# Optimization experiments

Measured on AMD Instinct MI355X. Metric: run time of the kernel, lower is better.

## Reference

```python
import jax, jax.numpy as jnp
import numpy as np

B, L = 128, 128            # batch, num_features (sequence length)
D_MODEL = 256
D_INNER = 512              # expand=2
D_STATE = 16
D_CONV = 4
DT_RANK = 16               # ceil(d_model/16)
N_LAYERS = 2
LN_EPS = 1e-5


def setup_inputs() -> dict:
    key = jax.random.key(0)
    ks = jax.random.split(key, 12)
    rn = lambda k, shp, s=0.02: (jax.random.normal(k, shp, jnp.float32) * s)
    A_init = jnp.tile(jnp.arange(1, D_STATE + 1, dtype=jnp.float32), (N_LAYERS, D_INNER, 1))
    return {
        "x_num": jax.random.normal(ks[0], (B, L), jnp.float32),
        "scalar_w": rn(ks[1], (D_MODEL, 1), 0.5),
        "scalar_b": jnp.zeros((D_MODEL,), jnp.float32),
        "in_proj_w": rn(ks[2], (N_LAYERS, 2 * D_INNER, D_MODEL)),
        "conv_w": rn(ks[3], (N_LAYERS, D_INNER, D_CONV), 0.2),
        "conv_b": jnp.zeros((N_LAYERS, D_INNER), jnp.float32),
        "x_proj_w": rn(ks[4], (N_LAYERS, DT_RANK + 2 * D_STATE, D_INNER)),
        "dt_proj_w": rn(ks[5], (N_LAYERS, D_INNER, DT_RANK), 0.1),
        "dt_proj_b": jnp.full((N_LAYERS, D_INNER), float(np.log(np.expm1(0.01))), jnp.float32),
        "A_log": jnp.log(A_init),
        "D_skip": jnp.ones((N_LAYERS, D_INNER), jnp.float32),
        "out_proj_w": rn(ks[6], (N_LAYERS, D_MODEL, D_INNER)),
        "ln_g": jnp.ones((D_MODEL,), jnp.float32),
        "ln_b": jnp.zeros((D_MODEL,), jnp.float32),
        "h1_w": rn(ks[7], (D_MODEL, D_MODEL)),
        "h1_b": jnp.zeros((D_MODEL,), jnp.float32),
        "h2_w": rn(ks[8], (1, D_MODEL)),
        "h2_b": jnp.zeros((1,), jnp.float32),
    }


def _selective_scan(u, delta, A, Bm, C, D_skip):
    # u, delta: [B,L,Di]; A: [Di,N]; Bm, C: [B,L,N]
    deltaA = jnp.exp(jnp.einsum('bld,dn->bldn', delta, A))          # [B,L,Di,N]
    deltaBu = jnp.einsum('bld,bln,bld->bldn', delta, Bm, u)          # [B,L,Di,N]
    h0 = jnp.zeros((u.shape[0], u.shape[2], A.shape[1]), u.dtype)

    def step(h, inp):
        dA_t, dBu_t, c_t = inp
        h = dA_t * h + dBu_t                                         # [B,Di,N]
        y = jnp.einsum('bdn,bn->bd', h, c_t)
        return h, y

    _, ys = jax.lax.scan(
        step, h0,
        (deltaA.transpose(1, 0, 2, 3), deltaBu.transpose(1, 0, 2, 3), C.transpose(1, 0, 2)))
    return ys.transpose(1, 0, 2) + u * D_skip                        # [B,L,Di]


def _mamba_block(x, Wi, cw, cb, Wx, Wdt, bdt, A_log, Dsk, Wo):
    xz = jnp.einsum('bld,ed->ble', x, Wi)                            # [B,L,2*Di]
    xh, z = jnp.split(xz, 2, axis=-1)
    # causal depthwise conv1d, kernel D_CONV
    xt = xh.transpose(0, 2, 1)                                       # [B,Di,L]
    conv = jax.lax.conv_general_dilated(
        xt, cw[:, None, :], window_strides=(1,), padding=[(D_CONV - 1, 0)],
        feature_group_count=D_INNER)
    xh = jax.nn.silu((conv + cb[:, None]).transpose(0, 2, 1))        # [B,L,Di]
    x_dbl = jnp.einsum('bld,ed->ble', xh, Wx)                        # [B,L,DT_RANK+2N]
    dt, Bm, C = jnp.split(x_dbl, [DT_RANK, DT_RANK + D_STATE], axis=-1)
    delta = jax.nn.softplus(jnp.einsum('blr,dr->bld', dt, Wdt) + bdt)
    A = -jnp.exp(A_log)
    y = _selective_scan(xh, delta, A, Bm, C, Dsk)
    y = y * jax.nn.silu(z)
    return jnp.einsum('bld,od->blo', y, Wo)                          # [B,L,D_MODEL]


def reference(x_num, scalar_w, scalar_b, in_proj_w, conv_w, conv_b, x_proj_w,
              dt_proj_w, dt_proj_b, A_log, D_skip, out_proj_w, ln_g, ln_b,
              h1_w, h1_b, h2_w, h2_b):
    # scalar_proj: Linear(1, d_model) applied to each feature value
    x = x_num[:, :, None] * scalar_w[:, 0] + scalar_b                # [B,L,D_MODEL]
    for i in range(N_LAYERS):
        x = _mamba_block(x, in_proj_w[i], conv_w[i], conv_b[i], x_proj_w[i],
                         dt_proj_w[i], dt_proj_b[i], A_log[i], D_skip[i], out_proj_w[i])
    mu = x.mean(-1, keepdims=True)
    var = ((x - mu) ** 2).mean(-1, keepdims=True)
    x = (x - mu) * jax.lax.rsqrt(var + LN_EPS) * ln_g + ln_b
    pooled = x.mean(axis=1)                                          # [B,D_MODEL]
    h = jax.nn.gelu(pooled @ h1_w.T + h1_b, approximate=False)
    return (h @ h2_w.T + h2_b)[:, 0]                                 # [B]
```

## Files before the change

### kernel.cpp

```cpp
#include <hip/hip_runtime.h>
#include <math.h>

#define BB 128
#define LL 128
#define DM 256
#define DI 512
#define NS 16
#define MR (BB*LL)
#define SC 8
#define ST 16
#define EPAD 34

typedef unsigned short u16;
typedef __attribute__((ext_vector_type(8))) short bf16x8;
typedef __attribute__((ext_vector_type(8))) short us8;
typedef __attribute__((ext_vector_type(4))) short u16x4;
typedef __attribute__((ext_vector_type(4))) float f32x4;
typedef __attribute__((ext_vector_type(2))) float f32x2;

__device__ __forceinline__ u16 f2bf(float v) {
    unsigned u = __float_as_uint(v);
    return (u16)((u + 0x7fffu + ((u >> 16) & 1u)) >> 16);
}
__device__ __forceinline__ u16 ftoh(float v) {
    _Float16 h = (_Float16)v;
    return __builtin_bit_cast(unsigned short, h);
}
__device__ __forceinline__ float htof(u16 x) {
    return (float)__builtin_bit_cast(_Float16, x);
}

__device__ __forceinline__ void g2l16(const u16* g, u16* l) {
    __builtin_amdgcn_global_load_lds(
        (const __attribute__((address_space(1))) void*)g,
        (__attribute__((address_space(3))) void*)l,
        16, 0, 0);
}

__device__ __forceinline__ void unpack8(const f32x4& a, const f32x4& b,
                                        const f32x4& c, const f32x4& d, f32x2* o) {
    o[0]=(f32x2){a[0],a[1]}; o[1]=(f32x2){a[2],a[3]};
    o[2]=(f32x2){b[0],b[1]}; o[3]=(f32x2){b[2],b[3]};
    o[4]=(f32x2){c[0],c[1]}; o[5]=(f32x2){c[2],c[3]};
    o[6]=(f32x2){d[0],d[1]}; o[7]=(f32x2){d[2],d[3]};
}

__device__ __forceinline__ void pow_tree2(float r, f32x2* p2) {
    float q = r*r, s = q*q, t = s*s;
    p2[0] = (f32x2){r, q};
    f32x2 qq = (f32x2){q, q}, ss = (f32x2){s, s}, tt = (f32x2){t, t};
    p2[1] = p2[0]*qq;
    p2[2] = p2[0]*ss;
    p2[3] = p2[1]*ss;
    p2[4] = p2[0]*tt;
    p2[5] = p2[1]*tt;
    p2[6] = p2[2]*tt;
    p2[7] = p2[3]*tt;
}

__device__ __forceinline__ void store8h(const float* v, u16* dh) {
    bf16x8 hv;
    #pragma unroll
    for (int j = 0; j < 8; j++) hv[j] = (short)f2bf(v[j]);
    *(bf16x8*)dh = hv;
}

__device__ __forceinline__ void unswz(int id, int NB, int& nb, int& mb) {
    int low = id & 7, rest = id >> 3;
    nb = rest % NB;
    mb = ((rest / NB) << 3) | low;
}

#define NCI (1024*32)
#define NCP (640*64)
#define NCO (256*64)
#define REG (NCI+NCP+NCO)
#define WSET 1441792
__global__ __launch_bounds__(256) void k_prep(
    const float* __restrict__ xn, const float* __restrict__ sw, const float* __restrict__ sbias,
    const float* __restrict__ Wi_all, const float* __restrict__ Wx_all,
    const float* __restrict__ Wdt_all, const float* __restrict__ Wo_all,
    u16* __restrict__ wbase, u16* __restrict__ AhA)
{
    int gc = blockIdx.x * 256 + threadIdx.x;
    if (gc < 2*REG) {
        int layer = (gc >= REG) ? 1 : 0;
        int c0 = gc - layer*REG;
        u16* wb = wbase + (size_t)layer*WSET;
        const float* Wi  = Wi_all  + (size_t)layer*1024*256;
        const float* Wx  = Wx_all  + (size_t)layer*48*512;
        const float* Wdt = Wdt_all + (size_t)layer*512*16;
        const float* Wo  = Wo_all  + (size_t)layer*256*512;
        float v[8];
        u16* dh;
        if (c0 < NCI) {
            int c = c0, m = c & 127, t = c >> 7, kc = t & 31, rb = t >> 5;
            const float* p = Wi + (size_t)(rb*128 + m)*256 + kc*8;
            float4 a = *(const float4*)p, b = *(const float4*)(p+4);
            v[0]=a.x; v[1]=a.y; v[2]=a.z; v[3]=a.w; v[4]=b.x; v[5]=b.y; v[6]=b.z; v[7]=b.w;
            dh = wb + (size_t)c*8;
        } else if (c0 < NCI + NCP) {
            int c = c0 - NCI, m = c & 127, t = c >> 7, kc = t & 63, rb = t >> 6;
            int row = rb*128 + m, k0 = kc*8;
            if (row < 512) {
                #pragma unroll
                for (int j = 0; j < 8; j++) v[j] = 0.f;
                #pragma unroll
                for (int r = 0; r < 16; r++) {
                    float wv = Wdt[row*16 + r];
                    const float* p = Wx + r*512 + k0;
                    #pragma unroll
                    for (int j = 0; j < 8; j++) v[j] += wv * p[j];
                }
            } else if (row < 544) {
                const float* p = Wx + (size_t)(row - 496)*512 + k0;
                #pragma unroll
                for (int j = 0; j < 8; j++) v[j] = p[j];
            } else {
                #pragma unroll
                for (int j = 0; j < 8; j++) v[j] = 0.f;
            }
            dh = wb + 524288 + (size_t)c*8;
        } else {
            int c = c0 - NCI - NCP, m = c & 127, t = c >> 7, kc = t & 63, rb = t >> 6;
            const float* p = Wo + (size_t)(rb*128 + m)*512 + kc*8;
            float4 a = *(const float4*)p, b = *(const float4*)(p+4);
            v[0]=a.x; v[1]=a.y; v[2]=a.z; v[3]=a.w; v[4]=b.x; v[5]=b.y; v[6]=b.z; v[7]=b.w;
            dh = wb + 1179648 + (size_t)c*8;
        }
        store8h(v, dh);
    } else {
        int id = gc - 2*REG;
        int row = id & (MR - 1);
        int kc  = id >> 14;
        float v = xn[row];
        float4 w0 = ((const float4*)sw)[kc*2],    w1 = ((const float4*)sw)[kc*2+1];
        float4 b0 = ((const float4*)sbias)[kc*2], b1 = ((const float4*)sbias)[kc*2+1];
        float vals[8] = { v*w0.x+b0.x, v*w0.y+b0.y, v*w0.z+b0.z, v*w0.w+b0.w,
                          v*w1.x+b1.x, v*w1.y+b1.y, v*w1.z+b1.z, v*w1.w+b1.w };
        size_t c = ((size_t)(row >> 7) * 32 + kc) * 128 + (row & 127);
        store8h(vals, &AhA[c*8]);
    }
}

template<int CM>
__global__ __launch_bounds__(256) void k_gemm_mfma(
    const u16* __restrict__ Ah, const u16* __restrict__ Bh,
    void* __restrict__ Cv, void* __restrict__ C2v,
    const float* __restrict__ bdt,
    int K, int Nvalid, int nsplit, int ldc, int ldc2, int NB)
{
    __shared__ __align__(16) u16 sAh[2][4*128*8];
    __shared__ __align__(16) u16 sBh[2][4*64*8];

    const int tid = threadIdx.x, lane = tid & 63, w = tid >> 6;
    const int wm = w >> 1, wn = w & 1;
    const int r16 = lane & 15, quad = lane >> 4;
    int nb, mb;
    unswz(blockIdx.x, NB, nb, mb);
    const int K8 = K >> 3;
    const int NT = K >> 5;

    f32x4 acc[4][2];
    #pragma unroll
    for (int mt = 0; mt < 4; mt++)
        #pragma unroll
        for (int nt = 0; nt < 2; nt++) acc[mt][nt] = (f32x4){0.f,0.f,0.f,0.f};

    const u16* gAh = Ah + (size_t)mb * K8 * 128 * 8;
    const int rbB = nb >> 1, boff = (nb & 1) * 64;
    const u16* gBh = Bh + (size_t)rbB * K8 * 128 * 8;

    {
        #pragma unroll
        for (int t = 0; t < 2; t++) {
            int s = w + t * 4;
            g2l16(gAh + (size_t)(s*64 + lane)*8, &sAh[0][(s*64 + lane)*8]);
        }
        g2l16(gBh + ((size_t)w*128 + boff + lane)*8, &sBh[0][(w*64 + lane)*8]);
    }

    int cur = 0;
    for (int t = 0; t < NT; t++) {
        __syncthreads();
        if (t + 1 < NT) {
            const int kc0 = (t + 1) * 4;
            const u16* ga = gAh + (size_t)kc0 * 128 * 8;
            int nx = cur ^ 1;
            #pragma unroll
            for (int tt = 0; tt < 2; tt++) {
                int s = w + tt * 4;
                g2l16(ga + (size_t)(s*64 + lane)*8, &sAh[nx][(s*64 + lane)*8]);
            }
            g2l16(gBh + ((size_t)(kc0 + w)*128 + boff + lane)*8, &sBh[nx][(w*64 + lane)*8]);
        }

        bf16x8 fa_h[4], fb_h[2];
        #pragma unroll
        for (int mt = 0; mt < 4; mt++) {
            int ch = quad*128 + wm*64 + mt*16 + r16;
            fa_h[mt] = *(const bf16x8*)&sAh[cur][ch*8];
        }
        #pragma unroll
        for (int nt = 0; nt < 2; nt++) {
            int ch = quad*64 + wn*32 + nt*16 + r16;
            fb_h[nt] = *(const bf16x8*)&sBh[cur][ch*8];
        }
        #pragma unroll
        for (int mt = 0; mt < 4; mt++)
            #pragma unroll
            for (int nt = 0; nt < 2; nt++)
                acc[mt][nt] = __builtin_amdgcn_mfma_f32_16x16x32_bf16(fa_h[mt], fb_h[nt], acc[mt][nt], 0, 0, 0);
        cur ^= 1;
    }

    const int col0 = nb*64 + wn*32;
    #pragma unroll
    for (int mt = 0; mt < 4; mt++) {
        int lrow = wm*64 + mt*16 + quad*4;
        int rowb = mb*128 + lrow;
        #pragma unroll
        for (int nt = 0; nt < 2; nt++) {
            int col = col0 + nt*16 + r16;
            if (col < Nvalid) {
                if (CM != 2 && col >= nsplit) {
                    float* Cd = (float*)C2v; int cc = col - nsplit;
                    #pragma unroll
                    for (int r = 0; r < 4; r++)
                        Cd[(size_t)(rowb + r)*ldc2 + cc] = acc[mt][nt][r];
                } else if (CM == 1) {
                    u16* Cd = (u16*)Cv;
                    float bv = bdt[col];
                    u16x4 pd;
                    #pragma unroll
                    for (int r = 0; r < 4; r++) {
                        float v    = acc[mt][nt][r] + bv;
                        float expv = __expf(v);
                        float dlt  = (v > 20.f) ? v : __logf(1.f + expv);
                        pd[r] = (short)ftoh(dlt);
                    }
                    *(u16x4*)&Cd[((size_t)mb*512 + col)*128 + lrow] = pd;
                } else if (CM == 2) {
                    u16* Dh = (u16*)Cv;
                    size_t cb = ((size_t)mb*32 + (col>>3))*1024 + (col&7);
                    #pragma unroll
                    for (int r = 0; r < 4; r++)
                        Dh[cb + (size_t)(lrow + r)*8] = f2bf(acc[mt][nt][r]);
                } else {
                    float* Cd = (float*)Cv;
                    #pragma unroll
                    for (int r = 0; r < 4; r++)
                        Cd[(size_t)(rowb + r)*ldc + col] = acc[mt][nt][r];
                }
            }
        }
    }
}

__global__ __launch_bounds__(256) void k_gemm_in(
    const u16* __restrict__ Ah, const u16* __restrict__ Bh,
    const float* __restrict__ cw, const float* __restrict__ cb,
    u16* __restrict__ Yh, u16* __restrict__ u2, u16* __restrict__ z2)
{
    __shared__ __align__(16) char smem[24576];
    u16* sAh = (u16*)smem;
    u16* sBh = (u16*)(smem + 16384);

    const int tid = threadIdx.x, lane = tid & 63, w = tid >> 6;
    const int wm = w >> 1, wn = w & 1;
    const int r16 = lane & 15, quad = lane >> 4;
    int nb, mb;
    unswz(blockIdx.x, 16, nb, mb);
    const int K8 = 32;
    const int NT = 8;

    f32x4 acc[4][2];
    #pragma unroll
    for (int mt = 0; mt < 4; mt++)
        #pragma unroll
        for (int nt = 0; nt < 2; nt++) acc[mt][nt] = (f32x4){0.f,0.f,0.f,0.f};

    const u16* gAh = Ah + (size_t)mb * K8 * 128 * 8;
    const int rbB = nb >> 1, boff = (nb & 1) * 64;
    const u16* gBh = Bh + (size_t)rbB * K8 * 128 * 8;

    {
        #pragma unroll
        for (int t = 0; t < 2; t++) {
            int s = w + t * 4;
            g2l16(gAh + (size_t)(s*64 + lane)*8, &sAh[(s*64 + lane)*8]);
        }
        g2l16(gBh + ((size_t)w*128 + boff + lane)*8, &sBh[(w*64 + lane)*8]);
    }

    int cur = 0;
    for (int t = 0; t < NT; t++) {
        __syncthreads();
        if (t + 1 < NT) {
            const int kc0 = (t + 1) * 4;
            const u16* ga = gAh + (size_t)kc0 * 128 * 8;
            u16* dA = sAh + (cur ^ 1) * 4096;
            u16* dB = sBh + (cur ^ 1) * 2048;
            #pragma unroll
            for (int tt = 0; tt < 2; tt++) {
                int s = w + tt * 4;
                g2l16(ga + (size_t)(s*64 + lane)*8, &dA[(s*64 + lane)*8]);
            }
            g2l16(gBh + ((size_t)(kc0 + w)*128 + boff + lane)*8, &dB[(w*64 + lane)*8]);
        }

        const u16* rA = sAh + cur * 4096;
        const u16* rB = sBh + cur * 2048;
        bf16x8 fa_h[4], fb_h[2];
        #pragma unroll
        for (int mt = 0; mt < 4; mt++) {
            int ch = quad*128 + wm*64 + mt*16 + r16;
            fa_h[mt] = *(const bf16x8*)&rA[ch*8];
        }
        #pragma unroll
        for (int nt = 0; nt < 2; nt++) {
            int ch = quad*64 + wn*32 + nt*16 + r16;
            fb_h[nt] = *(const bf16x8*)&rB[ch*8];
        }
        #pragma unroll
        for (int mt = 0; mt < 4; mt++)
            #pragma unroll
            for (int nt = 0; nt < 2; nt++)
                acc[mt][nt] = __builtin_amdgcn_mfma_f32_16x16x32_bf16(fa_h[mt], fb_h[nt], acc[mt][nt], 0, 0, 0);
        cur ^= 1;
    }

    if (nb < 8) {
        float* eps = (float*)smem;
        float* scw = (float*)(smem + 17408);
        float* scb = (float*)(smem + 18432);
        __syncthreads();
        if (tid < 256) scw[tid] = cw[nb*256 + tid];
        if (tid < 64)  scb[tid] = cb[nb*64 + tid];

        #pragma unroll
        for (int rr = 0; rr < 2; rr++) {
            if (wn == rr) {
                #pragma unroll
                for (int mt = 0; mt < 4; mt++) {
                    int rbase = wm*64 + mt*16 + quad*4;
                    #pragma unroll
                    for (int ntl = 0; ntl < 2; ntl++) {
                        int ct = ntl*16 + r16;
                        #pragma unroll
                        for (int r = 0; r < 4; r++)
                            eps[(rbase + r)*EPAD + ct] = acc[mt][ntl][r];
                    }
                }
            }
            __syncthreads();
            #pragma unroll
            for (int t = 0; t < 2; t++) {
                int l  = (tid & 31) + ((tid >> 5) & 3) * 32;
                int oo = (tid >> 7) + t*2;
                int dl_ = rr*32 + oo*8;
                float xr[4][8];
                #pragma unroll
                for (int r2 = 0; r2 < 4; r2++) {
                    int row = l - 3 + r2;
                    if (row >= 0) {
                        const float2* p = (const float2*)&eps[row*EPAD + oo*8];
                        float2 a = p[0], b2 = p[1], c2 = p[2], d2 = p[3];
                        xr[r2][0]=a.x; xr[r2][1]=a.y; xr[r2][2]=b2.x; xr[r2][3]=b2.y;
                        xr[r2][4]=c2.x; xr[r2][5]=c2.y; xr[r2][6]=d2.x; xr[r2][7]=d2.y;
                    } else {
                        #pragma unroll
                        for (int j = 0; j < 8; j++) xr[r2][j] = 0.f;
                    }
                }
                float uv[8];
                #pragma unroll
                for (int j = 0; j < 8; j++) {
                    int dj = dl_ + j;
                    float4 w4 = *(const float4*)&scw[dj*4];
                    float s = scb[dj] + w4.x*xr[0][j] + w4.y*xr[1][j]
                                      + w4.z*xr[2][j] + w4.w*xr[3][j];
                    float sig = 1.f/(1.f + __expf(-s));
                    uv[j] = s*sig;
                }
                int d = nb*64 + dl_;
                size_t base = ((size_t)(mb*64 + (d>>3))*128 + l)*8;
                store8h(uv, &Yh[base]);
                #pragma unroll
                for (int j = 0; j < 8; j++)
                    u2[((size_t)mb*512 + d + j)*128 + l] = ftoh(uv[j]);
            }
            __syncthreads();
        }
    } else {
        const int col0 = (nb-8)*64 + wn*32;
        #pragma unroll
        for (int mt = 0; mt < 4; mt++) {
            int lb = wm*64 + mt*16 + quad*4;
            #pragma unroll
            for (int nt = 0; nt < 2; nt++) {
                int d = col0 + nt*16 + r16;
                u16x4 pk;
                #pragma unroll
                for (int r = 0; r < 4; r++) pk[r] = (short)ftoh(acc[mt][nt][r]);
                *(u16x4*)&z2[((size_t)mb*512 + d)*128 + lb] = pk;
            }
        }
    }
}

__global__ __launch_bounds__(512, 8) void k_scan_fused(
    const u16* __restrict__ dls, const float* __restrict__ bc,
    const u16* __restrict__ uu, const u16* __restrict__ zz,
    const float* __restrict__ Dsk, u16* __restrict__ Yh)
{
    __shared__ float sR[SC][64];
    __shared__ float sH[SC][64*17];
    const int tid  = threadIdx.x;
    const int lane = tid & 63;
    const int c    = __builtin_amdgcn_readfirstlane(tid >> 6);
    const int dgrp = blockIdx.x & 7;
    const int b    = blockIdx.x >> 3;
    const int d    = dgrp*64 + lane;
    const int l0   = c*ST;

    const float dsk = Dsk[d];
    const size_t tb = ((size_t)b*512 + d)*128 + l0;
    const u16* pd = dls + tb;
    const u16* up = uu + tb;
    const u16* zp = zz + tb;
    const size_t ybase = ((size_t)(b*64 + (d>>3))*128 + l0)*8 + (d&7);
    const float* bp = bc + ((size_t)b*LL + l0)*32;

    f32x2 h2[8];
    #pragma unroll
    for (int n = 0; n < 8; n++) h2[n] = (f32x2){0.f, 0.f};
    float R = 1.f;

    #pragma unroll 1
    for (int t8 = 0; t8 < ST/8; t8++) {
        us8 vd = *(const us8*)(pd + t8*8);
        us8 vu = *(const us8*)(up + t8*8);
        #pragma unroll
        for (int j = 0; j < 8; j++) {
            int t = t8*8 + j;
            const float* bpt = bp + t*32;
            f32x4 qa = *(const f32x4*)(bpt);
            f32x4 qb = *(const f32x4*)(bpt + 4);
            f32x4 qc = *(const f32x4*)(bpt + 8);
            f32x4 qd = *(const f32x4*)(bpt + 12);
            f32x2 bvv[8];
            unpack8(qa, qb, qc, qd, bvv);
            float dlt = htof((u16)vd[j]);
            float r1  = __expf(-dlt);
            float du  = dlt * htof((u16)vu[j]);
            R *= r1;
            f32x2 p2[8];
            pow_tree2(r1, p2);
            f32x2 du2 = (f32x2){du, du};
            #pragma unroll
            for (int n = 0; n < 8; n++) h2[n] = p2[n]*h2[n] + bvv[n]*du2;
        }
    }

    sR[c][lane] = R;
    #pragma unroll
    for (int n = 0; n < 8; n++) {
        sH[c][lane*17 + 2*n]     = h2[n][0];
        sH[c][lane*17 + 2*n + 1] = h2[n][1];
    }
    __syncthreads();
    f32x2 hin2[8];
    #pragma unroll
    for (int n = 0; n < 8; n++) hin2[n] = (f32x2){0.f, 0.f};
    for (int cc = 0; cc < c; cc++) {
        float Rv = sR[cc][lane];
        f32x2 P2[8];
        pow_tree2(Rv, P2);
        #pragma unroll
        for (int n = 0; n < 8; n++) {
            f32x2 Sv = (f32x2){sH[cc][lane*17 + 2*n], sH[cc][lane*17 + 2*n + 1]};
            hin2[n] = P2[n]*hin2[n] + Sv;
        }
    }

    #pragma unroll
    for (int n = 0; n < 8; n++) h2[n] = hin2[n];

    u16* ph = Yh + ybase;

    #pragma unroll 1
    for (int t8 = 0; t8 < ST/8; t8++) {
        us8 vd = *(const us8*)(pd + t8*8);
        us8 vu = *(const us8*)(up + t8*8);
        us8 vz = *(const us8*)(zp + t8*8);
        #pragma unroll
        for (int j = 0; j < 8; j++) {
            int t = t8*8 + j;
            const float* bpt = bp + t*32;
            f32x4 qa = *(const f32x4*)(bpt);
            f32x4 qb = *(const f32x4*)(bpt + 4);
            f32x4 qc = *(const f32x4*)(bpt + 8);
            f32x4 qd = *(const f32x4*)(bpt + 12);
            f32x4 qe = *(const f32x4*)(bpt + 16);
            f32x4 qf = *(const f32x4*)(bpt + 20);
            f32x4 qg = *(const f32x4*)(bpt + 24);
            f32x4 qh = *(const f32x4*)(bpt + 28);
            f32x2 bvv[8], cvv[8];
            unpack8(qa, qb, qc, qd, bvv);
            unpack8(qe, qf, qg, qh, cvv);
            float dlt = htof((u16)vd[j]);
            float r1  = __expf(-dlt);
            float u   = htof((u16)vu[j]);
            float zv  = htof((u16)vz[j]);
            float du  = dlt * u;
            f32x2 p2[8];
            pow_tree2(r1, p2);
            f32x2 du2 = (f32x2){du, du};
            f32x2 yv2 = (f32x2){0.f, 0.f};
            #pragma unroll
            for (int n = 0; n < 8; n++) {
                h2[n] = p2[n]*h2[n] + bvv[n]*du2;
                yv2  += h2[n]*cvv[n];
            }
            float yv = yv2[0] + yv2[1] + u * dsk;
            float sig = 1.f/(1.f + __expf(-zv));
            float yg = yv * (zv * sig);
            ph[(size_t)t*8] = f2bf(yg);
        }
    }
}

__global__ __launch_bounds__(256) void k_ln_head(const float* __restrict__ x,
    const float* __restrict__ g, const float* __restrict__ bt,
    const float* __restrict__ h1w, const float* __restrict__ h1b,
    const float* __restrict__ h2w, const float* __restrict__ h2b,
    float* __restrict__ out)
{
    __shared__ float4 part[4][64];
    __shared__ float sp[DM];
    __shared__ float sred[DM];
    int b = blockIdx.x, tid = threadIdx.x, wave = tid >> 6, lane = tid & 63;
    const float4* xp = (const float4*)(x + (size_t)b*LL*DM);
    float4 acc = make_float4(0.f, 0.f, 0.f, 0.f);
    for (int i = 0; i < 32; i++) {
        int l = wave*32 + i;
        float4 v = xp[l*64 + lane];
        float s  = v.x + v.y + v.z + v.w;
        float s2 = v.x*v.x + v.y*v.y + v.z*v.z + v.w*v.w;
        #pragma unroll
        for (int off = 32; off > 0; off >>= 1) {
            s  += __shfl_down(s,  off, 64);
            s2 += __shfl_down(s2, off, 64);
        }
        s  = __shfl(s,  0, 64);
        s2 = __shfl(s2, 0, 64);
        float mu  = s  * (1.f/DM);
        float var = s2 * (1.f/DM) - mu*mu;
        float rs  = rsqrtf(var + 1e-5f);
        acc.x += (v.x - mu)*rs;
        acc.y += (v.y - mu)*rs;
        acc.z += (v.z - mu)*rs;
        acc.w += (v.w - mu)*rs;
    }
    part[wave][lane] = acc;
    __syncthreads();
    if (wave == 0) {
        float4 a0 = part[0][lane], a1 = part[1][lane], a2 = part[2][lane], a3 = part[3][lane];
        float4 gv = ((const float4*)g)[lane];
        float4 bv = ((const float4*)bt)[lane];
        float4 o;
        o.x = (a0.x+a1.x+a2.x+a3.x)*(1.f/LL)*gv.x + bv.x;
        o.y = (a0.y+a1.y+a2.y+a3.y)*(1.f/LL)*gv.y + bv.y;
        o.z = (a0.z+a1.z+a2.z+a3.z)*(1.f/LL)*gv.z + bv.z;
        o.w = (a0.w+a1.w+a2.w+a3.w)*(1.f/LL)*gv.w + bv.w;
        *(float4*)&sp[lane*4] = o;
    }
    __syncthreads();
    int j = tid;
    float a = h1b[j];
    const float* wr = &h1w[(size_t)j*DM];
    for (int m = 0; m < DM; m += 4) {
        float4 w4 = *(const float4*)&wr[m];
        a += sp[m]*w4.x + sp[m+1]*w4.y + sp[m+2]*w4.z + sp[m+3]*w4.w;
    }
    float hg = 0.5f*a*(1.f + erff(a*0.70710678118654752440f));
    sred[j] = hg * h2w[j];
    __syncthreads();
    for (int s = 128; s > 0; s >>= 1) {
        if (j < s) sred[j] += sred[j+s];
        __syncthreads();
    }
    if (j == 0) out[b] = sred[0] + h2b[0];
}

extern "C" void kernel_launch(void* const* d_in, const int* in_sizes, int n_in,
                              void* d_out, int out_size, void* d_ws, size_t ws_size,
                              hipStream_t stream)
{
    const float* x_num    = (const float*)d_in[0];
    const float* scalar_w = (const float*)d_in[1];
    const float* scalar_b = (const float*)d_in[2];
    const float* in_proj  = (const float*)d_in[3];
    const float* conv_w   = (const float*)d_in[4];
    const float* conv_b   = (const float*)d_in[5];
    const float* x_proj   = (const float*)d_in[6];
    const float* dt_w     = (const float*)d_in[7];
    const float* dt_b     = (const float*)d_in[8];
    const float* D_skip   = (const float*)d_in[10];
    const float* out_proj = (const float*)d_in[11];
    const float* ln_g     = (const float*)d_in[12];
    const float* ln_b     = (const float*)d_in[13];
    const float* h1_w     = (const float*)d_in[14];
    const float* h1_b     = (const float*)d_in[15];
    const float* h2_w     = (const float*)d_in[16];
    const float* h2_b     = (const float*)d_in[17];
    float* out = (float*)d_out;

    float* ws      = (float*)d_ws;
    float* x_buf   = ws;
    float* xh_raw  = x_buf  + (size_t)MR*DM;
    float* z_buf   = xh_raw + (size_t)MR*DI;
    float* xh      = z_buf  + (size_t)MR*DI;
    float* xdbl    = xh     + (size_t)MR*DI;
    float* wsplit  = xdbl   + (size_t)MR*48;

    u16* AhA = (u16*)xh;
    u16* u2  = (u16*)(xh + (size_t)MR*256);
    u16* AhX = (u16*)xh_raw;
    u16* z2  = (u16*)z_buf;
    u16* dl2 = (u16*)x_buf;
    float* bc = xdbl;

    u16* wbase = (u16*)wsplit;

    const int BIG = 1 << 30;

    k_prep<<<(2*REG + MR*32)/256, 256, 0, stream>>>(
        x_num, scalar_w, scalar_b, in_proj, x_proj, dt_w, out_proj,
        wbase, AhA);

    for (int layer = 0; layer < 2; layer++) {
        u16* wb  = wbase + (size_t)layer*WSET;
        u16* WhI = wb;
        u16* WhP = wb + 524288;
        u16* WhO = wb + 1179648;

        k_gemm_in<<<16*BB, 256, 0, stream>>>(
            AhA, WhI,
            conv_w + (size_t)layer*DI*4, conv_b + (size_t)layer*DI,
            AhX, u2, z2);

        k_gemm_mfma<1><<<9*BB, 256, 0, stream>>>(
            AhX, WhP, (void*)dl2, (void*)bc,
            dt_b + (size_t)layer*DI, 512, 544, 512, 512, 32, 9);

        k_scan_fused<<<BB*8, 512, 0, stream>>>(dl2, bc, u2, z2,
            D_skip + (size_t)layer*DI, AhX);

        if (layer == 0)
            k_gemm_mfma<2><<<4*BB, 256, 0, stream>>>(
                AhX, WhO, (void*)AhA, (void*)0, (const float*)0,
                512, 256, BIG, 256, 256, 4);
        else
            k_gemm_mfma<0><<<4*BB, 256, 0, stream>>>(
                AhX, WhO, x_buf, x_buf, (const float*)0,
                512, 256, BIG, 256, 256, 4);
    }

    k_ln_head<<<BB, 256, 0, stream>>>(x_buf, ln_g, ln_b, h1_w, h1_b, h2_w, h2_b, out);
}
```

Before: 314.8 us.

## Fold scalar projection into layer-0 in_proj and fuse out_proj0 into in_proj1

The layer-0 in_proj GEMM is replaced by a rank-1 closed form. Because the input is x*w+b, in_proj(x) = x*(Wi·w) + (Wi·b), so a new front kernel computes conv and SiLU directly from per-channel vectors. The layer-0 out_proj and the layer-1 in_proj are merged into a single 512-K GEMM with precomputed combined weights Wi1·Wo0, which removes one full activation GEMM pass. The cost is a small weight-weight GEMM per call and a change in bf16 rounding, since the combined weight product is rounded once instead of the intermediate activations.

```diff
diff --git a/kernel.cpp b/kernel.cpp
--- a/kernel.cpp
+++ b/kernel.cpp
@@ -74,72 +74,145 @@
 #define NCI (1024*32)
 #define NCP (640*64)
 #define NCO (256*64)
-#define REG (NCI+NCP+NCO)
-#define WSET 1441792
+#define NPREP (NCI + 2*NCP + 2*NCO + 256)
+#define OFF_WI1  0
+#define OFF_WP0  262144
+#define OFF_WP1  589824
+#define OFF_WO1  917504
+#define OFF_WOT0 1048576
 __global__ __launch_bounds__(256) void k_prep(
-    const float* __restrict__ xn, const float* __restrict__ sw, const float* __restrict__ sbias,
+    const float* __restrict__ sw, const float* __restrict__ sbias,
     const float* __restrict__ Wi_all, const float* __restrict__ Wx_all,
     const float* __restrict__ Wdt_all, const float* __restrict__ Wo_all,
-    u16* __restrict__ wbase, u16* __restrict__ AhA)
+    u16* __restrict__ wbase, float* __restrict__ wvbv)
 {
     int gc = blockIdx.x * 256 + threadIdx.x;
-    if (gc < 2*REG) {
-        int layer = (gc >= REG) ? 1 : 0;
-        int c0 = gc - layer*REG;
-        u16* wb = wbase + (size_t)layer*WSET;
-        const float* Wi  = Wi_all  + (size_t)layer*1024*256;
+    float v[8];
+    u16* dh;
+    if (gc < NCI) {
+        int c = gc, m = c & 127, t = c >> 7, kc = t & 31, rb = t >> 5;
+        const float* Wi = Wi_all + (size_t)1024*256;
+        const float* p = Wi + (size_t)(rb*128 + m)*256 + kc*8;
+        float4 a = *(const float4*)p, b = *(const float4*)(p+4);
+        v[0]=a.x; v[1]=a.y; v[2]=a.z; v[3]=a.w; v[4]=b.x; v[5]=b.y; v[6]=b.z; v[7]=b.w;
+        dh = wbase + OFF_WI1 + (size_t)c*8;
+    } else if (gc < NCI + 2*NCP) {
+        int g = gc - NCI;
+        int layer = (g >= NCP) ? 1 : 0;
+        int c = g - layer*NCP;
         const float* Wx  = Wx_all  + (size_t)layer*48*512;
         const float* Wdt = Wdt_all + (size_t)layer*512*16;
-        const float* Wo  = Wo_all  + (size_t)layer*256*512;
-        float v[8];
-        u16* dh;
-        if (c0 < NCI) {
-            int c = c0, m = c & 127, t = c >> 7, kc = t & 31, rb = t >> 5;
-            const float* p = Wi + (size_t)(rb*128 + m)*256 + kc*8;
-            float4 a = *(const float4*)p, b = *(const float4*)(p+4);
-            v[0]=a.x; v[1]=a.y; v[2]=a.z; v[3]=a.w; v[4]=b.x; v[5]=b.y; v[6]=b.z; v[7]=b.w;
-            dh = wb + (size_t)c*8;
-        } else if (c0 < NCI + NCP) {
-            int c = c0 - NCI, m = c & 127, t = c >> 7, kc = t & 63, rb = t >> 6;
-            int row = rb*128 + m, k0 = kc*8;
-            if (row < 512) {
+        int m = c & 127, t = c >> 7, kc = t & 63, rb = t >> 6;
+        int row = rb*128 + m, k0 = kc*8;
+        if (row < 512) {
+            #pragma unroll
+            for (int j = 0; j < 8; j++) v[j] = 0.f;
+            #pragma unroll
+            for (int r = 0; r < 16; r++) {
+                float wvx = Wdt[row*16 + r];
+                const float* p = Wx + r*512 + k0;
                 #pragma unroll
-                for (int j = 0; j < 8; j++) v[j] = 0.f;
-                #pragma unroll
-                for (int r = 0; r < 16; r++) {
-                    float wv = Wdt[row*16 + r];
-                    const float* p = Wx + r*512 + k0;
-                    #pragma unroll
-                    for (int j = 0; j < 8; j++) v[j] += wv * p[j];
-                }
-            } else if (row < 544) {
-                const float* p = Wx + (size_t)(row - 496)*512 + k0;
-                #pragma unroll
-                for (int j = 0; j < 8; j++) v[j] = p[j];
-            } else {
-                #pragma unroll
-                for (int j = 0; j < 8; j++) v[j] = 0.f;
-            }
-            dh = wb + 524288 + (size_t)c*8;
+                for (int j = 0; j < 8; j++) v[j] += wvx * p[j];
+            }
+        } else if (row < 544) {
+            const float* p = Wx + (size_t)(row - 496)*512 + k0;
+            #pragma unroll
+            for (int j = 0; j < 8; j++) v[j] = p[j];
         } else {
-            int c = c0 - NCI - NCP, m = c & 127, t = c >> 7, kc = t & 63, rb = t >> 6;
-            const float* p = Wo + (size_t)(rb*128 + m)*512 + kc*8;
-            float4 a = *(const float4*)p, b = *(const float4*)(p+4);
-            v[0]=a.x; v[1]=a.y; v[2]=a.z; v[3]=a.w; v[4]=b.x; v[5]=b.y; v[6]=b.z; v[7]=b.w;
-            dh = wb + 1179648 + (size_t)c*8;
-        }
-        store8h(v, dh);
+            #pragma unroll
+            for (int j = 0; j < 8; j++) v[j] = 0.f;
+        }
+        dh = wbase + (layer ? OFF_WP1 : OFF_WP0) + (size_t)c*8;
+    } else if (gc < NCI + 2*NCP + NCO) {
+        int c = gc - NCI - 2*NCP;
+        int m = c & 127, t = c >> 7, kc = t & 63, rb = t >> 6;
+        const float* Wo = Wo_all + (size_t)256*512;
+        const float* p = Wo + (size_t)(rb*128 + m)*512 + kc*8;
+        float4 a = *(const float4*)p, b = *(const float4*)(p+4);
+        v[0]=a.x; v[1]=a.y; v[2]=a.z; v[3]=a.w; v[4]=b.x; v[5]=b.y; v[6]=b.z; v[7]=b.w;
+        dh = wbase + OFF_WO1 + (size_t)c*8;
+    } else if (gc < NCI + 2*NCP + 2*NCO) {
+        int c = gc - NCI - 2*NCP - NCO;
+        int m = c & 127, t = c >> 7, kc = t & 31, rb = t >> 5;
+        int d = rb*128 + m;
+        const float* Wo = Wo_all;
+        #pragma unroll
+        for (int j = 0; j < 8; j++) v[j] = Wo[(size_t)(kc*8 + j)*512 + d];
+        dh = wbase + OFF_WOT0 + (size_t)c*8;
+    } else if (gc < NPREP) {
+        int j = gc - (NCI + 2*NCP + 2*NCO);
+        int isB = j >> 7;
+        int e0 = (j & 127) * 8;
+        const float* vec = isB ? sbias : sw;
+        const float* Wi0 = Wi_all;
+        float acc8[8];
+        #pragma unroll
+        for (int jj = 0; jj < 8; jj++) {
+            const float* row = Wi0 + (size_t)(e0 + jj)*256;
+            float a = 0.f;
+            for (int m = 0; m < 256; m += 4) {
+                float4 w4 = *(const float4*)&row[m];
+                float4 v4 = *(const float4*)&vec[m];
+                a += w4.x*v4.x + w4.y*v4.y + w4.z*v4.z + w4.w*v4.w;
+            }
+            acc8[jj] = a;
+        }
+        float* dst = wvbv + isB*1024 + e0;
+        *(float4*)dst       = make_float4(acc8[0], acc8[1], acc8[2], acc8[3]);
+        *(float4*)(dst + 4) = make_float4(acc8[4], acc8[5], acc8[6], acc8[7]);
+        return;
     } else {
-        int id = gc - 2*REG;
-        int row = id & (MR - 1);
-        int kc  = id >> 14;
-        float v = xn[row];
-        float4 w0 = ((const float4*)sw)[kc*2],    w1 = ((const float4*)sw)[kc*2+1];
-        float4 b0 = ((const float4*)sbias)[kc*2], b1 = ((const float4*)sbias)[kc*2+1];
-        float vals[8] = { v*w0.x+b0.x, v*w0.y+b0.y, v*w0.z+b0.z, v*w0.w+b0.w,
-                          v*w1.x+b1.x, v*w1.y+b1.y, v*w1.z+b1.z, v*w1.w+b1.w };
-        size_t c = ((size_t)(row >> 7) * 32 + kc) * 128 + (row & 127);
-        store8h(vals, &AhA[c*8]);
+        return;
+    }
+    store8h(v, dh);
+}
+
+__global__ __launch_bounds__(256) void k_front0(
+    const float* __restrict__ xn, const float* __restrict__ wvbv,
+    const float* __restrict__ cw, const float* __restrict__ cb,
+    u16* __restrict__ Yh, u16* __restrict__ u2, u16* __restrict__ z2)
+{
+    const int bid = blockIdx.x;
+    const int b = bid >> 3, seg = bid & 7;
+    const int tid = threadIdx.x;
+    const int l = tid & 127, sub = tid >> 7;
+    const float* xb = xn + (size_t)b * LL;
+    const float x0  = xb[l];
+    const float xm1 = (l >= 1) ? xb[l-1] : 0.f;
+    const float xm2 = (l >= 2) ? xb[l-2] : 0.f;
+    const float xm3 = (l >= 3) ? xb[l-3] : 0.f;
+    const float* wv = wvbv;
+    const float* bv = wvbv + 1024;
+    if (seg < 4) {
+        const int kcb = (seg*128 + sub*64) >> 3;
+        #pragma unroll 1
+        for (int kk = 0; kk < 8; kk++) {
+            const int kc = kcb + kk;
+            float uv[8];
+            #pragma unroll
+            for (int q = 0; q < 8; q++) {
+                int d = kc*8 + q;
+                float4 c4 = *(const float4*)&cw[d*4];
+                float conv = c4.x*xm3 + c4.y*xm2 + c4.z*xm1 + c4.w*x0;
+                float cs = c4.w;
+                if (l >= 1) cs += c4.z;
+                if (l >= 2) cs += c4.y;
+                if (l >= 3) cs += c4.x;
+                float s = wv[d]*conv + bv[d]*cs + cb[d];
+                float sig = 1.f/(1.f + __expf(-s));
+                uv[q] = s*sig;
+                u2[((size_t)b*512 + d)*128 + l] = ftoh(uv[q]);
+            }
+            store8h(uv, &Yh[(((size_t)b*64 + kc)*128 + l)*8]);
+        }
+    } else {
+        const int d0 = (seg - 4)*128 + sub*64;
+        #pragma unroll 1
+        for (int dd = 0; dd < 64; dd++) {
+            int d = d0 + dd;
+            float s = x0*wv[512 + d] + bv[512 + d];
+            z2[((size_t)b*512 + d)*128 + l] = ftoh(s);
+        }
     }
 }
 
@@ -242,7 +315,7 @@
                     *(u16x4*)&Cd[((size_t)mb*512 + col)*128 + lrow] = pd;
                 } else if (CM == 2) {
                     u16* Dh = (u16*)Cv;
-                    size_t cb = ((size_t)mb*32 + (col>>3))*1024 + (col&7);
+                    size_t cb = ((size_t)mb*(size_t)ldc + (col>>3))*1024 + (col&7);
                     #pragma unroll
                     for (int r = 0; r < 4; r++)
                         Dh[cb + (size_t)(lrow + r)*8] = f2bf(acc[mt][nt][r]);
@@ -260,7 +333,7 @@
 __global__ __launch_bounds__(256) void k_gemm_in(
     const u16* __restrict__ Ah, const u16* __restrict__ Bh,
     const float* __restrict__ cw, const float* __restrict__ cb,
-    u16* __restrict__ Yh, u16* __restrict__ u2, u16* __restrict__ z2)
+    u16* __restrict__ Yh, u16* __restrict__ u2, u16* __restrict__ z2, int K8c)
 {
     __shared__ __align__(16) char smem[24576];
     u16* sAh = (u16*)smem;
@@ -271,8 +344,7 @@
     const int r16 = lane & 15, quad = lane >> 4;
     int nb, mb;
     unswz(blockIdx.x, 16, nb, mb);
-    const int K8 = 32;
-    const int NT = 8;
+    const int NT = K8c >> 2;
 
     f32x4 acc[4][2];
     #pragma unroll
@@ -280,9 +352,9 @@
         #pragma unroll
         for (int nt = 0; nt < 2; nt++) acc[mt][nt] = (f32x4){0.f,0.f,0.f,0.f};
 
-    const u16* gAh = Ah + (size_t)mb * K8 * 128 * 8;
+    const u16* gAh = Ah + (size_t)mb * K8c * 128 * 8;
     const int rbB = nb >> 1, boff = (nb & 1) * 64;
-    const u16* gBh = Bh + (size_t)rbB * K8 * 128 * 8;
+    const u16* gBh = Bh + (size_t)rbB * K8c * 128 * 8;
 
     {
         #pragma unroll
@@ -625,48 +697,49 @@
     float* xdbl    = xh     + (size_t)MR*DI;
     float* wsplit  = xdbl   + (size_t)MR*48;
 
-    u16* AhA = (u16*)xh;
-    u16* u2  = (u16*)(xh + (size_t)MR*256);
-    u16* AhX = (u16*)xh_raw;
-    u16* z2  = (u16*)z_buf;
-    u16* dl2 = (u16*)x_buf;
+    u16* u2   = (u16*)(xh + (size_t)MR*256);
+    u16* AhX  = (u16*)xh_raw;
+    u16* z2   = (u16*)z_buf;
+    u16* Yh1  = (u16*)z_buf + (size_t)MR*512;
+    u16* dl2  = (u16*)x_buf;
     float* bc = xdbl;
 
-    u16* wbase = (u16*)wsplit;
+    u16* wbase   = (u16*)wsplit;
+    float* extra = wsplit + 589824;
+    u16* Wcomb   = (u16*)extra;
+    float* wvbv  = extra + 262144;
 
     const int BIG = 1 << 30;
 
-    k_prep<<<(2*REG + MR*32)/256, 256, 0, stream>>>(
-        x_num, scalar_w, scalar_b, in_proj, x_proj, dt_w, out_proj,
-        wbase, AhA);
-
-    for (int layer = 0; layer < 2; layer++) {
-        u16* wb  = wbase + (size_t)layer*WSET;
-        u16* WhI = wb;
-        u16* WhP = wb + 524288;
-        u16* WhO = wb + 1179648;
-
-        k_gemm_in<<<16*BB, 256, 0, stream>>>(
-            AhA, WhI,
-            conv_w + (size_t)layer*DI*4, conv_b + (size_t)layer*DI,
-            AhX, u2, z2);
-
-        k_gemm_mfma<1><<<9*BB, 256, 0, stream>>>(
-            AhX, WhP, (void*)dl2, (void*)bc,
-            dt_b + (size_t)layer*DI, 512, 544, 512, 512, 32, 9);
-
-        k_scan_fused<<<BB*8, 512, 0, stream>>>(dl2, bc, u2, z2,
-            D_skip + (size_t)layer*DI, AhX);
-
-        if (layer == 0)
-            k_gemm_mfma<2><<<4*BB, 256, 0, stream>>>(
-                AhX, WhO, (void*)AhA, (void*)0, (const float*)0,
-                512, 256, BIG, 256, 256, 4);
-        else
-            k_gemm_mfma<0><<<4*BB, 256, 0, stream>>>(
-                AhX, WhO, x_buf, x_buf, (const float*)0,
-                512, 256, BIG, 256, 256, 4);
-    }
+    k_prep<<<NPREP/256, 256, 0, stream>>>(
+        scalar_w, scalar_b, in_proj, x_proj, dt_w, out_proj, wbase, wvbv);
+
+    k_gemm_mfma<2><<<64, 256, 0, stream>>>(
+        wbase + OFF_WI1, wbase + OFF_WOT0, (void*)Wcomb, (void*)0, (const float*)0,
+        256, 512, BIG, 64 , 0, 8);
+
+    k_front0<<<BB*8, 256, 0, stream>>>(
+        x_num, wvbv, conv_w, conv_b, AhX, u2, z2);
+
+    k_gemm_mfma<1><<<9*BB, 256, 0, stream>>>(
+        AhX, wbase + OFF_WP0, (void*)dl2, (void*)bc,
+        dt_b, 512, 544, 512, 512, 32, 9);
+
+    k_scan_fused<<<BB*8, 512, 0, stream>>>(dl2, bc, u2, z2, D_skip, AhX);
+
+    k_gemm_in<<<16*BB, 256, 0, stream>>>(
+        AhX, Wcomb, conv_w + (size_t)DI*4, conv_b + DI,
+        Yh1, u2, z2, 64);
+
+    k_gemm_mfma<1><<<9*BB, 256, 0, stream>>>(
+        Yh1, wbase + OFF_WP1, (void*)dl2, (void*)bc,
+        dt_b + DI, 512, 544, 512, 512, 32, 9);
+
+    k_scan_fused<<<BB*8, 512, 0, stream>>>(dl2, bc, u2, z2, D_skip + DI, AhX);
+
+    k_gemm_mfma<0><<<4*BB, 256, 0, stream>>>(
+        AhX, wbase + OFF_WO1, (void*)x_buf, (void*)x_buf, (const float*)0,
+        512, 256, BIG, 256, 256, 4);
 
     k_ln_head<<<BB, 256, 0, stream>>>(x_buf, ln_g, ln_b, h1_w, h1_b, h2_w, h2_b, out);
 }
```

After: 402.9 us. 1.28x slower.
